# Kernel tuning notes

Hardware: AMD Instinct MI355X
Metric: run time of the kernel (lower is better)

The kernel has to match this reference:

```python
import jax, jax.numpy as jnp
import numpy as np

N, D, H, C = 16384, 2048, 512, 65
EPS_LOG = 1e-6   # matches torch log(p + 1e-6)
EPS_NORM = 1e-12 # matches F.normalize default eps


def setup_inputs() -> dict:
    key = jax.random.key(0)
    k0, k1, k2 = jax.random.split(key, 3)
    return {
        "feat": jax.random.normal(k0, (N, D), jnp.float32),
        "w1": jax.random.normal(k1, (D, H), jnp.float32) * (1.0 / np.sqrt(D)),
        "b1": jnp.zeros((H,), jnp.float32),
        "w2": jax.random.normal(k2, (H, C), jnp.float32) * (1.0 / np.sqrt(H)),
        "b2": jnp.zeros((C,), jnp.float32),
    }


def reference(feat, w1, b1, w2, b2):
    n, c = feat.shape[0], w2.shape[1]
    # fc1 -> relu -> dropout(p=0.5, training=True; fixed key for determinism) -> fc2
    h = jax.nn.relu(feat @ w1 + b1)
    keep = jax.random.bernoulli(jax.random.key(42), 0.5, h.shape)
    h = jnp.where(keep, h * 2.0, 0.0)
    logits = h @ w2 + b2

    logp = jax.nn.log_softmax(logits, axis=1)
    p = jnp.exp(logp)  # softmax_out

    entropy = -jnp.mean(jnp.sum(p * jnp.log(p + EPS_LOG), axis=1))
    mean_p = jnp.mean(p, axis=0)
    diversity = jnp.sum(mean_p * jnp.log(mean_p + EPS_LOG))

    # per-class centroids: one-pass segment reduce instead of python loop over classes
    pseudo_preds = jnp.argmax(p, axis=1)
    sums = jax.ops.segment_sum(feat, pseudo_preds, num_segments=c)          # [C, D]
    counts = jax.ops.segment_sum(jnp.ones((n,), feat.dtype), pseudo_preds, num_segments=c)
    means = sums / jnp.maximum(counts, 1.0)[:, None]
    norms = jnp.linalg.norm(means, axis=1, keepdims=True)
    centroids = jnp.where(counts[:, None] > 0, means / jnp.maximum(norms, EPS_NORM), 0.0)

    feat_n = feat / jnp.maximum(jnp.linalg.norm(feat, axis=1, keepdims=True), EPS_NORM)
    sim = feat_n @ centroids.T                                              # [N, C]
    pseudo_labels = jnp.argmax(sim, axis=1)

    ce = -jnp.mean(jnp.take_along_axis(logp, pseudo_labels[:, None], axis=1))
    loss = entropy + diversity + 0.3 * ce
    return loss
```

## Files before the change

kernel.cpp:

```cpp
#include <hip/hip_runtime.h>

typedef unsigned short us;
typedef unsigned int u32;
typedef __attribute__((ext_vector_type(8))) short short8;
typedef __attribute__((ext_vector_type(4))) float f32x4;

#define MFMA16(a, b, c) __builtin_amdgcn_mfma_f32_16x16x32_bf16((a), (b), (c), 0, 0, 0)

#define GLD16(lptr, gptr) __builtin_amdgcn_global_load_lds( \
    (__attribute__((address_space(1))) void*)(gptr), \
    (__attribute__((address_space(3))) void*)(lptr), 16, 0, 0)

__device__ inline us f2bf(float f) {
  u32 u = __float_as_uint(f);
  u32 r = (u + 0x7FFFu + ((u >> 16) & 1u)) >> 16;
  return (us)r;
}
__device__ inline float bf2f(us s) { return __uint_as_float((u32)s << 16); }
__device__ inline void splitbf(float x, us& hi, us& lo) {
  hi = f2bf(x);
  lo = f2bf(x - bf2f(hi));
}

__global__ void k_init(float* accs, int* cnt, int* cursor) {
  int t = threadIdx.x;
  if (t < 68) accs[t] = 0.f;
  if (t < 65) { cnt[t] = 0; cursor[t] = 0; }
}

#define TF_R(a) { x0 += x1; x1 = (x1 << (a)) | (x1 >> (32 - (a))); x1 ^= x0; }
__global__ void k_mask(u32* __restrict__ mask) {
  u32 t = blockIdx.x * 256u + threadIdx.x;
  const u32 K0 = 0u, K1 = 42u, K2 = 0x1BD11BDAu ^ 0u ^ 42u;
  u32 w0 = 0, w1 = 0;
  for (int i = 0; i < 32; ++i) {
    u32 x0 = t * 32u + (u32)i;
    u32 x1 = x0 + 4194304u;
    x0 += K0; x1 += K1;
    TF_R(13) TF_R(15) TF_R(26) TF_R(6)   x0 += K1; x1 += K2 + 1u;
    TF_R(17) TF_R(29) TF_R(16) TF_R(24)  x0 += K2; x1 += K0 + 2u;
    TF_R(13) TF_R(15) TF_R(26) TF_R(6)   x0 += K0; x1 += K1 + 3u;
    TF_R(17) TF_R(29) TF_R(16) TF_R(24)  x0 += K1; x1 += K2 + 4u;
    TF_R(13) TF_R(15) TF_R(26) TF_R(6)   x0 += K2; x1 += K0 + 5u;
    w0 |= (u32)((x0 >> 31) == 0u) << i;
    w1 |= (u32)((x1 >> 31) == 0u) << i;
  }
  mask[t] = w0;
  mask[t + 131072u] = w1;
}

__global__ void k_splitw1(const float* __restrict__ w1, us* __restrict__ th, us* __restrict__ tl) {
  __shared__ float tile[64][65];
  int k0 = blockIdx.x * 64, n0 = blockIdx.y * 64;
  int t = threadIdx.x;
  int cr = t >> 6, cc = t & 63;
  for (int i = 0; i < 16; ++i) {
    int r = i * 4 + cr;
    tile[r][cc] = w1[(size_t)(k0 + r) * 512 + n0 + cc];
  }
  __syncthreads();
  for (int i = 0; i < 16; ++i) {
    int n = i * 4 + cr;
    int k = cc;
    us hi, lo; splitbf(tile[k][n], hi, lo);
    size_t o = (size_t)(n0 + n) * 2048 + k0 + k;
    th[o] = hi; tl[o] = lo;
  }
}

__global__ void k_splitw2(const float* __restrict__ w2, us* __restrict__ th, us* __restrict__ tl) {
  int n = blockIdx.x;
  for (int k = threadIdx.x; k < 512; k += 256) {
    float v = (n < 65) ? w2[(size_t)k * 65 + n] : 0.f;
    us hi, lo; splitbf(v, hi, lo);
    th[n * 512 + k] = hi; tl[n * 512 + k] = lo;
  }
}

__global__ void k_splitfeat(const float* __restrict__ x, us* __restrict__ xh, us* __restrict__ xl) {
  size_t g = ((size_t)blockIdx.x * 256 + threadIdx.x) * 8;
  f32x4 a = *(const f32x4*)(x + g);
  f32x4 b = *(const f32x4*)(x + g + 4);
  short8 h8, l8;
  for (int i = 0; i < 4; ++i) {
    us hi, lo;
    splitbf(a[i], hi, lo); h8[i] = (short)hi; l8[i] = (short)lo;
    splitbf(b[i], hi, lo); h8[4 + i] = (short)hi; l8[4 + i] = (short)lo;
  }
  *(short8*)(xh + g) = h8;
  *(short8*)(xl + g) = l8;
}

__global__ __launch_bounds__(256, 2) void k_gemm1(
    const us* __restrict__ Ah_, const us* __restrict__ Al_,
    const us* __restrict__ Bh_, const us* __restrict__ Bl_,
    const float* __restrict__ b1, const u32* __restrict__ mask,
    us* __restrict__ Hh, us* __restrict__ Hl) {
  __shared__ __align__(16) us lds[4 * 8192];
  us* sAh = lds; us* sAl = lds + 8192; us* sBh = lds + 16384; us* sBl = lds + 24576;
  int tid = threadIdx.x;
  int bm = blockIdx.x, bn = blockIdx.y;
  int m0 = bm * 128, n0 = bn * 128;
  int lane = tid & 63, wv = tid >> 6;
  int wm = (wv >> 1) * 64, wn = (wv & 1) * 64;
  int frow = lane & 15, fq = lane >> 4;
  int srow = tid >> 3;
  int scolsw = (((tid & 7) ^ ((tid >> 3) & 7)) * 8);
  f32x4 acc[4][4] = {};
  size_t arow = (size_t)(m0 + srow) * 2048 + scolsw;
  size_t brow = (size_t)(n0 + srow) * 2048 + scolsw;
  for (int kt = 0; kt < 32; ++kt) {
    int k0 = kt * 64;
    __syncthreads();
#pragma unroll
    for (int j = 0; j < 4; ++j) {
      int lo = j * 2048 + wv * 512;
      size_t go = (size_t)j * 32 * 2048 + k0;
      GLD16(sAh + lo, Ah_ + arow + go);
      GLD16(sAl + lo, Al_ + arow + go);
      GLD16(sBh + lo, Bh_ + brow + go);
      GLD16(sBl + lo, Bl_ + brow + go);
    }
    __syncthreads();
#pragma unroll
    for (int s = 0; s < 2; ++s) {
      short8 ah[4], al[4], bh[4], bl[4];
#pragma unroll
      for (int f = 0; f < 4; ++f) {
        int ca = ((s * 4 + fq) ^ (frow & 7)) * 8;
        int ra = (wm + f * 16 + frow) * 64 + ca;
        int rb = (wn + f * 16 + frow) * 64 + ca;
        ah[f] = *(const short8*)&sAh[ra];
        al[f] = *(const short8*)&sAl[ra];
        bh[f] = *(const short8*)&sBh[rb];
        bl[f] = *(const short8*)&sBl[rb];
      }
#pragma unroll
      for (int i = 0; i < 4; ++i)
#pragma unroll
        for (int j2 = 0; j2 < 4; ++j2) {
          acc[i][j2] = MFMA16(ah[i], bh[j2], acc[i][j2]);
          acc[i][j2] = MFMA16(ah[i], bl[j2], acc[i][j2]);
          acc[i][j2] = MFMA16(al[i], bh[j2], acc[i][j2]);
        }
    }
  }
#pragma unroll
  for (int i = 0; i < 4; ++i)
#pragma unroll
    for (int j = 0; j < 4; ++j)
#pragma unroll
      for (int r = 0; r < 4; ++r) {
        int row = m0 + wm + i * 16 + (lane >> 4) * 4 + r;
        int col = n0 + wn + j * 16 + (lane & 15);
        float v = acc[i][j][r] + b1[col];
        v = fmaxf(v, 0.f);
        u32 f = (u32)row * 512u + (u32)col;
        u32 keep = (mask[f >> 5] >> (f & 31u)) & 1u;
        v = keep ? v * 2.f : 0.f;
        us hi, lo; splitbf(v, hi, lo);
        size_t o = (size_t)row * 512 + col;
        Hh[o] = hi; Hl[o] = lo;
      }
}

__global__ __launch_bounds__(256, 2) void k_gemm2(
    const us* __restrict__ Ah_, const us* __restrict__ Al_,
    const us* __restrict__ Bh_, const us* __restrict__ Bl_,
    const float* __restrict__ b2,
    float* __restrict__ logp, int* __restrict__ preds,
    float* __restrict__ accs ) {
  __shared__ __align__(16) us sA[2][4096];
  __shared__ __align__(16) us sB[2][5120];
  __shared__ float slog[64 * 81];
  __shared__ float sm[64], sl[64];
  __shared__ float sred[256];
  int tid = threadIdx.x;
  int m0 = blockIdx.x * 64;
  int lane = tid & 63, wv = tid >> 6;
  int frow = lane & 15, fq = lane >> 4;
  int srow = tid >> 3;
  int scolsw = (((tid & 7) ^ ((tid >> 3) & 7)) * 8);
  f32x4 acc[5] = {};
  size_t arow = (size_t)(m0 + srow) * 512 + scolsw;
  size_t brow = (size_t)srow * 512 + scolsw;
  size_t brow2 = (size_t)(64 + (tid >> 3)) * 512 + scolsw;
  for (int kt = 0; kt < 8; ++kt) {
    int k0 = kt * 64;
    __syncthreads();
#pragma unroll
    for (int j = 0; j < 2; ++j) {
      int lo = j * 2048 + wv * 512;
      size_t go = (size_t)j * 32 * 512 + k0;
      GLD16(&sA[0][lo], Ah_ + arow + go);
      GLD16(&sA[1][lo], Al_ + arow + go);
      GLD16(&sB[0][lo], Bh_ + brow + go);
      GLD16(&sB[1][lo], Bl_ + brow + go);
    }
    if (wv < 2) {
      GLD16(&sB[0][4096 + wv * 512], Bh_ + brow2 + k0);
      GLD16(&sB[1][4096 + wv * 512], Bl_ + brow2 + k0);
    }
    __syncthreads();
#pragma unroll
    for (int s = 0; s < 2; ++s) {
      int ca = ((s * 4 + fq) ^ (frow & 7)) * 8;
      short8 a_h = *(const short8*)&sA[0][(wv * 16 + frow) * 64 + ca];
      short8 a_l = *(const short8*)&sA[1][(wv * 16 + frow) * 64 + ca];
#pragma unroll
      for (int fn = 0; fn < 5; ++fn) {
        short8 b_h = *(const short8*)&sB[0][(fn * 16 + frow) * 64 + ca];
        short8 b_l = *(const short8*)&sB[1][(fn * 16 + frow) * 64 + ca];
        acc[fn] = MFMA16(a_h, b_h, acc[fn]);
        acc[fn] = MFMA16(a_h, b_l, acc[fn]);
        acc[fn] = MFMA16(a_l, b_h, acc[fn]);
      }
    }
  }
#pragma unroll
  for (int fn = 0; fn < 5; ++fn) {
    int col = fn * 16 + (lane & 15);
    if (col < 65) {
      float bb = b2[col];
#pragma unroll
      for (int r = 0; r < 4; ++r) {
        int row = wv * 16 + (lane >> 4) * 4 + r;
        slog[row * 81 + col] = acc[fn][r] + bb;
      }
    }
  }
  __syncthreads();
  if (tid < 64) {
    int row = tid;
    float m = -1e30f; int am = 0;
    for (int c = 0; c < 65; ++c) {
      float v = slog[row * 81 + c];
      if (v > m) { m = v; am = c; }
    }
    float s = 0.f;
    for (int c = 0; c < 65; ++c) s += expf(slog[row * 81 + c] - m);
    sm[row] = m; sl[row] = logf(s);
    preds[m0 + row] = am;
  }
  __syncthreads();
  float entp = 0.f;
  if (tid < 240) {
    int c = tid % 80, rr0 = tid / 80;
    if (c < 65) {
      float mpp = 0.f;
      for (int r = rr0; r < 64; r += 3) {
        float v = slog[r * 81 + c] - sm[r] - sl[r];
        logp[(size_t)(m0 + r) * 65 + c] = v;
        float p = expf(v);
        mpp += p;
        entp += p * logf(p + 1e-6f);
      }
      atomicAdd(&accs[2 + c], mpp);
    }
  }
  sred[tid] = entp;
  __syncthreads();
  for (int s = 128; s > 0; s >>= 1) { if (tid < s) sred[tid] += sred[tid + s]; __syncthreads(); }
  if (tid == 0) atomicAdd(&accs[0], sred[0]);
}

__global__ __launch_bounds__(256) void k_hist(const int* __restrict__ preds, int* __restrict__ cnt) {
  __shared__ int h[65];
  int tid = threadIdx.x;
  if (tid < 65) h[tid] = 0;
  __syncthreads();
  int i = blockIdx.x * 256 + tid;
  atomicAdd(&h[preds[i]], 1);
  __syncthreads();
  if (tid < 65 && h[tid] > 0) atomicAdd(&cnt[tid], h[tid]);
}

__global__ void k_scan(const int* __restrict__ cnt, int* __restrict__ base) {
  if (threadIdx.x == 0) {
    int s = 0;
    for (int c = 0; c < 65; ++c) { base[c] = s; s += cnt[c]; }
  }
}

__global__ __launch_bounds__(256) void k_scatter(
    const int* __restrict__ preds, const int* __restrict__ base,
    int* __restrict__ cursor, int* __restrict__ rowidx) {
  __shared__ int h[65];
  __shared__ int gb[65];
  int tid = threadIdx.x;
  if (tid < 65) h[tid] = 0;
  __syncthreads();
  int i = blockIdx.x * 256 + tid;
  int c = preds[i];
  int pos = atomicAdd(&h[c], 1);
  __syncthreads();
  if (tid < 65 && h[tid] > 0) gb[tid] = atomicAdd(&cursor[tid], h[tid]);
  __syncthreads();
  rowidx[base[c] + gb[c] + pos] = i;
}

__global__ __launch_bounds__(256) void k_segsum2(
    const float* __restrict__ feat, const int* __restrict__ rowidx,
    const int* __restrict__ base, const int* __restrict__ cnt,
    float* __restrict__ psum ) {
  int c = blockIdx.x;
  int j = blockIdx.y;
  int tid = threadIdx.x;
  int start = base[c], n = cnt[c];
  f32x4 a0 = {}, a1 = {};
  const float* fp = feat + (size_t)tid * 8;
  for (int i = j; i < n; i += 8) {
    int row = rowidx[start + i];
    const f32x4* p = (const f32x4*)(fp + (size_t)row * 2048);
    a0 += p[0];
    a1 += p[1];
  }
  float* o = psum + ((size_t)(j * 65 + c)) * 2048 + (size_t)tid * 8;
  *(f32x4*)o = a0;
  *(f32x4*)(o + 4) = a1;
}

__global__ __launch_bounds__(256) void k_centroid(
    const float* __restrict__ psum, const int* __restrict__ pcnt,
    us* __restrict__ ch, us* __restrict__ cl) {
  int c = blockIdx.x;
  int tid = threadIdx.x;
  if (c >= 65) {
    for (int d = tid; d < 2048; d += 256) { ch[(size_t)c * 2048 + d] = 0; cl[(size_t)c * 2048 + d] = 0; }
    return;
  }
  int cnt = pcnt[c];
  float inv = 1.0f / (float)((cnt > 1) ? cnt : 1);
  float mean[8]; float sq = 0.f;
  for (int i = 0; i < 8; ++i) {
    int d = tid + i * 256;
    float s = 0.f;
    for (int nc = 0; nc < 8; ++nc) s += psum[((size_t)nc * 65 + c) * 2048 + d];
    mean[i] = s * inv;
    sq += mean[i] * mean[i];
  }
  __shared__ float red[256];
  red[tid] = sq; __syncthreads();
  for (int s = 128; s > 0; s >>= 1) { if (tid < s) red[tid] += red[tid + s]; __syncthreads(); }
  float norm = sqrtf(red[0]);
  float dscale = (cnt > 0) ? 1.0f / fmaxf(norm, 1e-12f) : 0.0f;
  for (int i = 0; i < 8; ++i) {
    int d = tid + i * 256;
    us hi, lo; splitbf(mean[i] * dscale, hi, lo);
    ch[(size_t)c * 2048 + d] = hi; cl[(size_t)c * 2048 + d] = lo;
  }
}

__global__ __launch_bounds__(256, 2) void k_sim(
    const us* __restrict__ Ah_, const us* __restrict__ Al_,
    const us* __restrict__ Bh_, const us* __restrict__ Bl_,
    float* __restrict__ simbuf ) {
  __shared__ __align__(16) us sA[2][4096];
  __shared__ __align__(16) us sB[2][5120];
  int tid = threadIdx.x;
  int m0 = blockIdx.x * 64;
  int ks = blockIdx.y;
  int kbase = ks * 1024;
  int lane = tid & 63, wv = tid >> 6;
  int frow = lane & 15, fq = lane >> 4;
  int srow = tid >> 3;
  int scolsw = (((tid & 7) ^ ((tid >> 3) & 7)) * 8);
  f32x4 acc[5] = {};
  size_t arow = (size_t)(m0 + srow) * 2048 + kbase + scolsw;
  size_t brow = (size_t)srow * 2048 + kbase + scolsw;
  size_t brow2 = (size_t)(64 + (tid >> 3)) * 2048 + kbase + scolsw;
  for (int kt = 0; kt < 16; ++kt) {
    int k0 = kt * 64;
    __syncthreads();
#pragma unroll
    for (int j = 0; j < 2; ++j) {
      int lo = j * 2048 + wv * 512;
      size_t go = (size_t)j * 32 * 2048 + k0;
      GLD16(&sA[0][lo], Ah_ + arow + go);
      GLD16(&sA[1][lo], Al_ + arow + go);
      GLD16(&sB[0][lo], Bh_ + brow + go);
      GLD16(&sB[1][lo], Bl_ + brow + go);
    }
    if (wv < 2) {
      GLD16(&sB[0][4096 + wv * 512], Bh_ + brow2 + k0);
      GLD16(&sB[1][4096 + wv * 512], Bl_ + brow2 + k0);
    }
    __syncthreads();
#pragma unroll
    for (int s = 0; s < 2; ++s) {
      int ca = ((s * 4 + fq) ^ (frow & 7)) * 8;
      short8 a_h = *(const short8*)&sA[0][(wv * 16 + frow) * 64 + ca];
      short8 a_l = *(const short8*)&sA[1][(wv * 16 + frow) * 64 + ca];
#pragma unroll
      for (int fn = 0; fn < 5; ++fn) {
        short8 b_h = *(const short8*)&sB[0][(fn * 16 + frow) * 64 + ca];
        short8 b_l = *(const short8*)&sB[1][(fn * 16 + frow) * 64 + ca];
        acc[fn] = MFMA16(a_h, b_h, acc[fn]);
        acc[fn] = MFMA16(a_h, b_l, acc[fn]);
        acc[fn] = MFMA16(a_l, b_h, acc[fn]);
      }
    }
  }
#pragma unroll
  for (int fn = 0; fn < 5; ++fn) {
    int col = fn * 16 + (lane & 15);
#pragma unroll
    for (int r = 0; r < 4; ++r) {
      int row = wv * 16 + (lane >> 4) * 4 + r;
      simbuf[((size_t)(ks * 16384 + m0 + row)) * 80 + col] = acc[fn][r];
    }
  }
}

__global__ __launch_bounds__(256) void k_simred(
    const float* __restrict__ simbuf, const float* __restrict__ logp,
    float* __restrict__ accs ) {
  __shared__ float sred[256];
  int tid = threadIdx.x;
  int row = blockIdx.x * 256 + tid;
  const float* p0 = simbuf + (size_t)row * 80;
  const float* p1 = simbuf + (size_t)(16384 + row) * 80;
  float m = -1e30f; int am = 0;
  for (int c = 0; c < 65; ++c) {
    float v = p0[c] + p1[c];
    if (v > m) { m = v; am = c; }
  }
  sred[tid] = logp[(size_t)row * 65 + am];
  __syncthreads();
  for (int s = 128; s > 0; s >>= 1) { if (tid < s) sred[tid] += sred[tid + s]; __syncthreads(); }
  if (tid == 0) atomicAdd(&accs[1], sred[0]);
}

__global__ void k_final(const float* __restrict__ accs, float* __restrict__ out) {
  __shared__ float red[256];
  int t = threadIdx.x;
  float d = 0.f;
  if (t < 65) {
    float mp = accs[2 + t] * (1.f / 16384.f);
    d = mp * logf(mp + 1e-6f);
  }
  red[t] = d; __syncthreads();
  for (int s = 128; s > 0; s >>= 1) { if (t < s) red[t] += red[t + s]; __syncthreads(); }
  if (t == 0) {
    float entropy = -accs[0] * (1.f / 16384.f);
    float ce = -accs[1] * (1.f / 16384.f);
    out[0] = entropy + red[0] + 0.3f * ce;
  }
}

extern "C" void kernel_launch(void* const* d_in, const int* in_sizes, int n_in,
                              void* d_out, int out_size, void* d_ws, size_t ws_size,
                              hipStream_t stream) {
  const float* feat = (const float*)d_in[0];
  const float* w1   = (const float*)d_in[1];
  const float* b1   = (const float*)d_in[2];
  const float* w2   = (const float*)d_in[3];
  const float* b2   = (const float*)d_in[4];
  float* out = (float*)d_out;

  char* w = (char*)d_ws;
  auto alloc = [&](size_t b) { char* p = w; w += (b + 255) & ~(size_t)255; return p; };
  us*  feat_hi = (us*)alloc(16384ull * 2048 * 2);
  us*  feat_lo = (us*)alloc(16384ull * 2048 * 2);
  us*  w1t_hi  = (us*)alloc(512ull * 2048 * 2);
  us*  w1t_lo  = (us*)alloc(512ull * 2048 * 2);
  us*  w2t_hi  = (us*)alloc(80ull * 512 * 2);
  us*  w2t_lo  = (us*)alloc(80ull * 512 * 2);
  u32* mask    = (u32*)alloc(262144ull * 4);
  us*  h_hi    = (us*)alloc(16384ull * 512 * 2);
  us*  h_lo    = (us*)alloc(16384ull * 512 * 2);
  float* logp  = (float*)alloc(16384ull * 65 * 4);
  int*   preds = (int*)alloc(16384ull * 4);
  float* psum  = (float*)alloc(8ull * 65 * 2048 * 4);
  int*   cnt   = (int*)alloc(65ull * 4);
  int*   base  = (int*)alloc(65ull * 4);
  int*   cursor= (int*)alloc(65ull * 4);
  int*   rowidx= (int*)alloc(16384ull * 4);
  us*  cent_hi = (us*)alloc(80ull * 2048 * 2);
  us*  cent_lo = (us*)alloc(80ull * 2048 * 2);
  float* simbuf= (float*)alloc(2ull * 16384 * 80 * 4);
  float* accs  = (float*)alloc(68ull * 4);

  k_init<<<1, 256, 0, stream>>>(accs, cnt, cursor);
  k_mask<<<512, 256, 0, stream>>>(mask);
  k_splitw1<<<dim3(32, 8), 256, 0, stream>>>(w1, w1t_hi, w1t_lo);
  k_splitw2<<<80, 256, 0, stream>>>(w2, w2t_hi, w2t_lo);
  k_splitfeat<<<16384, 256, 0, stream>>>(feat, feat_hi, feat_lo);
  k_gemm1<<<dim3(128, 4), 256, 0, stream>>>(feat_hi, feat_lo, w1t_hi, w1t_lo, b1, mask, h_hi, h_lo);
  k_gemm2<<<256, 256, 0, stream>>>(h_hi, h_lo, w2t_hi, w2t_lo, b2, logp, preds, accs);
  k_hist<<<64, 256, 0, stream>>>(preds, cnt);
  k_scan<<<1, 64, 0, stream>>>(cnt, base);
  k_scatter<<<64, 256, 0, stream>>>(preds, base, cursor, rowidx);
  k_segsum2<<<dim3(65, 8), 256, 0, stream>>>(feat, rowidx, base, cnt, psum);
  k_centroid<<<80, 256, 0, stream>>>(psum, cnt, cent_hi, cent_lo);
  k_sim<<<dim3(256, 2), 256, 0, stream>>>(feat_hi, feat_lo, cent_hi, cent_lo, simbuf);
  k_simred<<<64, 256, 0, stream>>>(simbuf, logp, accs);
  k_final<<<1, 256, 0, stream>>>(accs, out);
}
```

Before: 534.6 us.

## Merge prep kernels, fold histogram/scan/final into neighbours to cut launches

```diff
diff --git a/kernel.cpp b/kernel.cpp
--- a/kernel.cpp
+++ b/kernel.cpp
@@ -22,73 +22,74 @@
   lo = f2bf(x - bf2f(hi));
 }
 
-__global__ void k_init(float* accs, int* cnt, int* cursor) {
-  int t = threadIdx.x;
-  if (t < 68) accs[t] = 0.f;
-  if (t < 65) { cnt[t] = 0; cursor[t] = 0; }
-}
-
 #define TF_R(a) { x0 += x1; x1 = (x1 << (a)) | (x1 >> (32 - (a))); x1 ^= x0; }
-__global__ void k_mask(u32* __restrict__ mask) {
-  u32 t = blockIdx.x * 256u + threadIdx.x;
-  const u32 K0 = 0u, K1 = 42u, K2 = 0x1BD11BDAu ^ 0u ^ 42u;
-  u32 w0 = 0, w1 = 0;
-  for (int i = 0; i < 32; ++i) {
-    u32 x0 = t * 32u + (u32)i;
-    u32 x1 = x0 + 4194304u;
-    x0 += K0; x1 += K1;
-    TF_R(13) TF_R(15) TF_R(26) TF_R(6)   x0 += K1; x1 += K2 + 1u;
-    TF_R(17) TF_R(29) TF_R(16) TF_R(24)  x0 += K2; x1 += K0 + 2u;
-    TF_R(13) TF_R(15) TF_R(26) TF_R(6)   x0 += K0; x1 += K1 + 3u;
-    TF_R(17) TF_R(29) TF_R(16) TF_R(24)  x0 += K1; x1 += K2 + 4u;
-    TF_R(13) TF_R(15) TF_R(26) TF_R(6)   x0 += K2; x1 += K0 + 5u;
-    w0 |= (u32)((x0 >> 31) == 0u) << i;
-    w1 |= (u32)((x1 >> 31) == 0u) << i;
-  }
-  mask[t] = w0;
-  mask[t + 131072u] = w1;
-}
-
-__global__ void k_splitw1(const float* __restrict__ w1, us* __restrict__ th, us* __restrict__ tl) {
+__global__ __launch_bounds__(256) void k_prep(
+    const float* __restrict__ feat, const float* __restrict__ w1, const float* __restrict__ w2,
+    us* __restrict__ xh, us* __restrict__ xl,
+    us* __restrict__ w1h, us* __restrict__ w1l,
+    us* __restrict__ w2h, us* __restrict__ w2l,
+    u32* __restrict__ mask, float* __restrict__ accs,
+    int* __restrict__ cnt, int* __restrict__ cursor, int* __restrict__ done) {
   __shared__ float tile[64][65];
-  int k0 = blockIdx.x * 64, n0 = blockIdx.y * 64;
-  int t = threadIdx.x;
-  int cr = t >> 6, cc = t & 63;
-  for (int i = 0; i < 16; ++i) {
-    int r = i * 4 + cr;
-    tile[r][cc] = w1[(size_t)(k0 + r) * 512 + n0 + cc];
-  }
-  __syncthreads();
-  for (int i = 0; i < 16; ++i) {
-    int n = i * 4 + cr;
-    int k = cc;
-    us hi, lo; splitbf(tile[k][n], hi, lo);
-    size_t o = (size_t)(n0 + n) * 2048 + k0 + k;
-    th[o] = hi; tl[o] = lo;
-  }
-}
-
-__global__ void k_splitw2(const float* __restrict__ w2, us* __restrict__ th, us* __restrict__ tl) {
-  int n = blockIdx.x;
-  for (int k = threadIdx.x; k < 512; k += 256) {
-    float v = (n < 65) ? w2[(size_t)k * 65 + n] : 0.f;
-    us hi, lo; splitbf(v, hi, lo);
-    th[n * 512 + k] = hi; tl[n * 512 + k] = lo;
-  }
-}
-
-__global__ void k_splitfeat(const float* __restrict__ x, us* __restrict__ xh, us* __restrict__ xl) {
-  size_t g = ((size_t)blockIdx.x * 256 + threadIdx.x) * 8;
-  f32x4 a = *(const f32x4*)(x + g);
-  f32x4 b = *(const f32x4*)(x + g + 4);
-  short8 h8, l8;
-  for (int i = 0; i < 4; ++i) {
-    us hi, lo;
-    splitbf(a[i], hi, lo); h8[i] = (short)hi; l8[i] = (short)lo;
-    splitbf(b[i], hi, lo); h8[4 + i] = (short)hi; l8[4 + i] = (short)lo;
-  }
-  *(short8*)(xh + g) = h8;
-  *(short8*)(xl + g) = l8;
+  int b = blockIdx.x, t = threadIdx.x;
+  if (b < 16384) {
+    size_t g = ((size_t)b * 256 + t) * 8;
+    f32x4 a = *(const f32x4*)(feat + g);
+    f32x4 bb = *(const f32x4*)(feat + g + 4);
+    short8 h8, l8;
+    for (int i = 0; i < 4; ++i) {
+      us hi, lo;
+      splitbf(a[i], hi, lo); h8[i] = (short)hi; l8[i] = (short)lo;
+      splitbf(bb[i], hi, lo); h8[4 + i] = (short)hi; l8[4 + i] = (short)lo;
+    }
+    *(short8*)(xh + g) = h8;
+    *(short8*)(xl + g) = l8;
+  } else if (b < 16896) {
+    u32 tt = (u32)(b - 16384) * 256u + (u32)t;
+    const u32 K0 = 0u, K1 = 42u, K2 = 0x1BD11BDAu ^ 0u ^ 42u;
+    u32 w0 = 0, w1r = 0;
+    for (int i = 0; i < 32; ++i) {
+      u32 x0 = tt * 32u + (u32)i;
+      u32 x1 = x0 + 4194304u;
+      x0 += K0; x1 += K1;
+      TF_R(13) TF_R(15) TF_R(26) TF_R(6)   x0 += K1; x1 += K2 + 1u;
+      TF_R(17) TF_R(29) TF_R(16) TF_R(24)  x0 += K2; x1 += K0 + 2u;
+      TF_R(13) TF_R(15) TF_R(26) TF_R(6)   x0 += K0; x1 += K1 + 3u;
+      TF_R(17) TF_R(29) TF_R(16) TF_R(24)  x0 += K1; x1 += K2 + 4u;
+      TF_R(13) TF_R(15) TF_R(26) TF_R(6)   x0 += K2; x1 += K0 + 5u;
+      w0 |= (u32)((x0 >> 31) == 0u) << i;
+      w1r |= (u32)((x1 >> 31) == 0u) << i;
+    }
+    mask[tt] = w0;
+    mask[tt + 131072u] = w1r;
+  } else if (b < 17152) {
+    int i = b - 16896;
+    int k0 = (i & 31) * 64, n0 = (i >> 5) * 64;
+    int cr = t >> 6, cc = t & 63;
+    for (int j = 0; j < 16; ++j) {
+      int r = j * 4 + cr;
+      tile[r][cc] = w1[(size_t)(k0 + r) * 512 + n0 + cc];
+    }
+    __syncthreads();
+    for (int j = 0; j < 16; ++j) {
+      int n = j * 4 + cr;
+      int k = cc;
+      us hi, lo; splitbf(tile[k][n], hi, lo);
+      size_t o = (size_t)(n0 + n) * 2048 + k0 + k;
+      w1h[o] = hi; w1l[o] = lo;
+    }
+  } else if (b < 17232) {
+    int n = b - 17152;
+    for (int k = t; k < 512; k += 256) {
+      float v = (n < 65) ? w2[(size_t)k * 65 + n] : 0.f;
+      us hi, lo; splitbf(v, hi, lo);
+      w2h[n * 512 + k] = hi; w2l[n * 512 + k] = lo;
+    }
+  } else {
+    if (t < 68) accs[t] = 0.f;
+    if (t < 65) { cnt[t] = 0; cursor[t] = 0; }
+    if (t == 0) done[0] = 0;
+  }
 }
 
 __global__ __launch_bounds__(256, 2) void k_gemm1(
@@ -169,12 +170,13 @@
     const us* __restrict__ Bh_, const us* __restrict__ Bl_,
     const float* __restrict__ b2,
     float* __restrict__ logp, int* __restrict__ preds,
-    float* __restrict__ accs ) {
+    float* __restrict__ accs , int* __restrict__ cnt) {
   __shared__ __align__(16) us sA[2][4096];
   __shared__ __align__(16) us sB[2][5120];
   __shared__ float slog[64 * 81];
   __shared__ float sm[64], sl[64];
   __shared__ float sred[256];
+  __shared__ int hh[65];
   int tid = threadIdx.x;
   int m0 = blockIdx.x * 64;
   int lane = tid & 63, wv = tid >> 6;
@@ -229,6 +231,7 @@
       }
     }
   }
+  if (tid < 65) hh[tid] = 0;
   __syncthreads();
   if (tid < 64) {
     int row = tid;
@@ -241,8 +244,10 @@
     for (int c = 0; c < 65; ++c) s += expf(slog[row * 81 + c] - m);
     sm[row] = m; sl[row] = logf(s);
     preds[m0 + row] = am;
-  }
-  __syncthreads();
+    atomicAdd(&hh[am], 1);
+  }
+  __syncthreads();
+  if (tid < 65 && hh[tid] > 0) atomicAdd(&cnt[tid], hh[tid]);
   float entp = 0.f;
   if (tid < 240) {
     int c = tid % 80, rr0 = tid / 80;
@@ -264,49 +269,38 @@
   if (tid == 0) atomicAdd(&accs[0], sred[0]);
 }
 
-__global__ __launch_bounds__(256) void k_hist(const int* __restrict__ preds, int* __restrict__ cnt) {
-  __shared__ int h[65];
-  int tid = threadIdx.x;
-  if (tid < 65) h[tid] = 0;
-  __syncthreads();
-  int i = blockIdx.x * 256 + tid;
-  atomicAdd(&h[preds[i]], 1);
-  __syncthreads();
-  if (tid < 65 && h[tid] > 0) atomicAdd(&cnt[tid], h[tid]);
-}
-
-__global__ void k_scan(const int* __restrict__ cnt, int* __restrict__ base) {
-  if (threadIdx.x == 0) {
-    int s = 0;
-    for (int c = 0; c < 65; ++c) { base[c] = s; s += cnt[c]; }
-  }
-}
-
 __global__ __launch_bounds__(256) void k_scatter(
-    const int* __restrict__ preds, const int* __restrict__ base,
+    const int* __restrict__ preds, const int* __restrict__ cnt,
     int* __restrict__ cursor, int* __restrict__ rowidx) {
   __shared__ int h[65];
   __shared__ int gb[65];
-  int tid = threadIdx.x;
-  if (tid < 65) h[tid] = 0;
+  __shared__ int sbase[65];
+  int tid = threadIdx.x;
+  if (tid < 65) { h[tid] = 0; sbase[tid] = cnt[tid]; }
   __syncthreads();
   int i = blockIdx.x * 256 + tid;
   int c = preds[i];
   int pos = atomicAdd(&h[c], 1);
+  if (tid == 0) {
+    int s = 0;
+    for (int cc = 0; cc < 65; ++cc) { int v = sbase[cc]; sbase[cc] = s; s += v; }
+  }
   __syncthreads();
   if (tid < 65 && h[tid] > 0) gb[tid] = atomicAdd(&cursor[tid], h[tid]);
   __syncthreads();
-  rowidx[base[c] + gb[c] + pos] = i;
+  rowidx[sbase[c] + gb[c] + pos] = i;
 }
 
 __global__ __launch_bounds__(256) void k_segsum2(
     const float* __restrict__ feat, const int* __restrict__ rowidx,
-    const int* __restrict__ base, const int* __restrict__ cnt,
+    const int* __restrict__ cnt,
     float* __restrict__ psum ) {
   int c = blockIdx.x;
   int j = blockIdx.y;
   int tid = threadIdx.x;
-  int start = base[c], n = cnt[c];
+  int start = 0;
+  for (int cc = 0; cc < 65; ++cc) { if (cc == c) break; start += cnt[cc]; }
+  int n = cnt[c];
   f32x4 a0 = {}, a1 = {};
   const float* fp = feat + (size_t)tid * 8;
   for (int i = j; i < n; i += 8) {
@@ -414,8 +408,9 @@
 
 __global__ __launch_bounds__(256) void k_simred(
     const float* __restrict__ simbuf, const float* __restrict__ logp,
-    float* __restrict__ accs ) {
+    float* __restrict__ accs, int* __restrict__ done, float* __restrict__ out) {
   __shared__ float sred[256];
+  __shared__ int lastflag;
   int tid = threadIdx.x;
   int row = blockIdx.x * 256 + tid;
   const float* p0 = simbuf + (size_t)row * 80;
@@ -428,23 +423,26 @@
   sred[tid] = logp[(size_t)row * 65 + am];
   __syncthreads();
   for (int s = 128; s > 0; s >>= 1) { if (tid < s) sred[tid] += sred[tid + s]; __syncthreads(); }
-  if (tid == 0) atomicAdd(&accs[1], sred[0]);
-}
-
-__global__ void k_final(const float* __restrict__ accs, float* __restrict__ out) {
-  __shared__ float red[256];
-  int t = threadIdx.x;
+  if (tid == 0) {
+    atomicAdd(&accs[1], sred[0]);
+    __threadfence();
+    int old = atomicAdd(done, 1);
+    lastflag = (old == 63);
+  }
+  __syncthreads();
+  if (!lastflag) return;
   float d = 0.f;
-  if (t < 65) {
-    float mp = accs[2 + t] * (1.f / 16384.f);
+  if (tid < 65) {
+    float mp = atomicAdd(&accs[2 + tid], 0.f) * (1.f / 16384.f);
     d = mp * logf(mp + 1e-6f);
   }
-  red[t] = d; __syncthreads();
-  for (int s = 128; s > 0; s >>= 1) { if (t < s) red[t] += red[t + s]; __syncthreads(); }
-  if (t == 0) {
-    float entropy = -accs[0] * (1.f / 16384.f);
-    float ce = -accs[1] * (1.f / 16384.f);
-    out[0] = entropy + red[0] + 0.3f * ce;
+  sred[tid] = d;
+  __syncthreads();
+  for (int s = 128; s > 0; s >>= 1) { if (tid < s) sred[tid] += sred[tid + s]; __syncthreads(); }
+  if (tid == 0) {
+    float entropy = -atomicAdd(&accs[0], 0.f) * (1.f / 16384.f);
+    float ce = -atomicAdd(&accs[1], 0.f) * (1.f / 16384.f);
+    out[0] = entropy + sred[0] + 0.3f * ce;
   }
 }
 
@@ -473,27 +471,22 @@
   int*   preds = (int*)alloc(16384ull * 4);
   float* psum  = (float*)alloc(8ull * 65 * 2048 * 4);
   int*   cnt   = (int*)alloc(65ull * 4);
-  int*   base  = (int*)alloc(65ull * 4);
   int*   cursor= (int*)alloc(65ull * 4);
   int*   rowidx= (int*)alloc(16384ull * 4);
   us*  cent_hi = (us*)alloc(80ull * 2048 * 2);
   us*  cent_lo = (us*)alloc(80ull * 2048 * 2);
   float* simbuf= (float*)alloc(2ull * 16384 * 80 * 4);
   float* accs  = (float*)alloc(68ull * 4);
-
-  k_init<<<1, 256, 0, stream>>>(accs, cnt, cursor);
-  k_mask<<<512, 256, 0, stream>>>(mask);
-  k_splitw1<<<dim3(32, 8), 256, 0, stream>>>(w1, w1t_hi, w1t_lo);
-  k_splitw2<<<80, 256, 0, stream>>>(w2, w2t_hi, w2t_lo);
-  k_splitfeat<<<16384, 256, 0, stream>>>(feat, feat_hi, feat_lo);
+  int*   done  = (int*)alloc(4ull);
+
+  k_prep<<<17233, 256, 0, stream>>>(feat, w1, w2, feat_hi, feat_lo,
+                                    w1t_hi, w1t_lo, w2t_hi, w2t_lo,
+                                    mask, accs, cnt, cursor, done);
   k_gemm1<<<dim3(128, 4), 256, 0, stream>>>(feat_hi, feat_lo, w1t_hi, w1t_lo, b1, mask, h_hi, h_lo);
-  k_gemm2<<<256, 256, 0, stream>>>(h_hi, h_lo, w2t_hi, w2t_lo, b2, logp, preds, accs);
-  k_hist<<<64, 256, 0, stream>>>(preds, cnt);
-  k_scan<<<1, 64, 0, stream>>>(cnt, base);
-  k_scatter<<<64, 256, 0, stream>>>(preds, base, cursor, rowidx);
-  k_segsum2<<<dim3(65, 8), 256, 0, stream>>>(feat, rowidx, base, cnt, psum);
+  k_gemm2<<<256, 256, 0, stream>>>(h_hi, h_lo, w2t_hi, w2t_lo, b2, logp, preds, accs, cnt);
+  k_scatter<<<64, 256, 0, stream>>>(preds, cnt, cursor, rowidx);
+  k_segsum2<<<dim3(65, 8), 256, 0, stream>>>(feat, rowidx, cnt, psum);
   k_centroid<<<80, 256, 0, stream>>>(psum, cnt, cent_hi, cent_lo);
   k_sim<<<dim3(256, 2), 256, 0, stream>>>(feat_hi, feat_lo, cent_hi, cent_lo, simbuf);
-  k_simred<<<64, 256, 0, stream>>>(simbuf, logp, accs);
-  k_final<<<1, 256, 0, stream>>>(accs, out);
-}
+  k_simred<<<64, 256, 0, stream>>>(simbuf, logp, accs, done, out);
+}
```

New measurement: 486.3 us. 9.0% less time.
